# Optimization experiments

Hardware: AMD Instinct MI355X
Metric: run time of the kernel (lower is better)

Reference implementation:

```python
import jax, jax.numpy as jnp
import numpy as np

B, T, D = 8, 1024, 768
H, HD = 12, 64
DFF = 3072
EPS = 1e-5


def setup_inputs() -> dict:
    key = jax.random.key(0)
    ks = jax.random.split(key, 6)
    s = lambda fan_in: 1.0 / np.sqrt(fan_in)
    return {
        "x": jax.random.normal(ks[0], (B, T, D), jnp.float32),
        "ln1_g": jnp.ones((D,), jnp.float32),
        "ln1_b": jnp.zeros((D,), jnp.float32),
        "w_qkv": jax.random.normal(ks[1], (D, 3 * D), jnp.float32) * s(D),
        "b_qkv": jnp.zeros((3 * D,), jnp.float32),
        "w_out": jax.random.normal(ks[2], (D, D), jnp.float32) * s(D),
        "b_out": jnp.zeros((D,), jnp.float32),
        "ln2_g": jnp.ones((D,), jnp.float32),
        "ln2_b": jnp.zeros((D,), jnp.float32),
        "w_fc1": jax.random.normal(ks[3], (D, DFF), jnp.float32) * s(D),
        "b_fc1": jnp.zeros((DFF,), jnp.float32),
        "w_fc2": jax.random.normal(ks[4], (DFF, D), jnp.float32) * s(DFF),
        "b_fc2": jnp.zeros((D,), jnp.float32),
    }


def _layernorm(x, g, b):
    mu = jnp.mean(x, axis=-1, keepdims=True)
    var = jnp.var(x, axis=-1, keepdims=True)
    return (x - mu) * jax.lax.rsqrt(var + EPS) * g + b


def reference(x, ln1_g, ln1_b, w_qkv, b_qkv, w_out, b_out,
              ln2_g, ln2_b, w_fc1, b_fc1, w_fc2, b_fc2):
    # --- attention branch (pre-norm) ---
    h = _layernorm(x, ln1_g, ln1_b)
    qkv = h @ w_qkv + b_qkv                      # [B,T,3D]
    q, k, v = jnp.split(qkv, 3, axis=-1)
    # [B,T,D] -> [B,H,T,HD]
    re = lambda t: t.reshape(B, T, H, HD).transpose(0, 2, 1, 3)
    q, k, v = re(q), re(k), re(v)
    scores = jnp.einsum("bhqd,bhkd->bhqk", q, k) * (1.0 / np.sqrt(HD))
    causal = jnp.tril(jnp.ones((T, T), bool))    # [T,T]
    scores = jnp.where(causal, scores, -jnp.inf)
    attn_weights = jax.nn.softmax(scores, axis=-1)  # [B,H,T,T]
    out = jnp.einsum("bhqk,bhkd->bhqd", attn_weights, v)
    out = out.transpose(0, 2, 1, 3).reshape(B, T, D)
    attn_out = out @ w_out + b_out
    x = x + attn_out
    # --- MLP branch (pre-norm) ---
    h2 = _layernorm(x, ln2_g, ln2_b)
    ff = jax.nn.gelu(h2 @ w_fc1 + b_fc1, approximate=False) @ w_fc2 + b_fc2
    x = x + ff
    return x, attn_weights
```

## Files before the change

kernel.cpp:

```cpp
#include <hip/hip_runtime.h>
#include <cstdint>
#include <cstddef>

namespace {

constexpr int Bb  = 8;
constexpr int Tt  = 1024;
constexpr int Dd  = 768;
constexpr int Hh  = 12;
constexpr int DFF = 3072;
constexpr int BT  = Bb * Tt;

typedef __attribute__((ext_vector_type(8))) short bf16x8;
typedef __attribute__((ext_vector_type(4))) short bf16x4;
typedef __attribute__((ext_vector_type(4))) float f32x4;

__device__ __forceinline__ short f2bf(float f) {
  union { float f; unsigned u; } v; v.f = f;
  unsigned r = v.u + 0x7fffu + ((v.u >> 16) & 1u);
  return (short)(r >> 16);
}
__device__ __forceinline__ float gelu_exact(float v) {
  return 0.5f * v * (1.0f + erff(v * 0.70710678118654752f));
}

#define MFMA16(a, b, c) __builtin_amdgcn_mfma_f32_16x16x32_bf16(a, b, c, 0, 0, 0)

__device__ __forceinline__ void gl_lds16(const short* g, short* l) {
  __builtin_amdgcn_global_load_lds(
      (const __attribute__((address_space(1))) unsigned int*)(g),
      (__attribute__((address_space(3))) unsigned int*)(l), 16, 0, 0);
}

__global__ __launch_bounds__(256) void cvt_t(const float* __restrict__ in,
                                             short* __restrict__ out,
                                             int K, int N) {
  __shared__ float tile[32][33];
  int k0 = blockIdx.x * 32, n0 = blockIdx.y * 32;
  int tx = threadIdx.x & 31, ty = threadIdx.x >> 5;
  #pragma unroll
  for (int r = ty; r < 32; r += 8)
    tile[r][tx] = in[(size_t)(k0 + r) * N + n0 + tx];
  __syncthreads();
  #pragma unroll
  for (int r = ty; r < 32; r += 8)
    out[(size_t)(n0 + r) * K + k0 + tx] = f2bf(tile[tx][r]);
}

__global__ __launch_bounds__(256) void ln_rows(const float* __restrict__ x,
                                               const float* __restrict__ g,
                                               const float* __restrict__ b,
                                               short* __restrict__ out) {
  int lane = threadIdx.x & 63, wid = threadIdx.x >> 6;
  int row = blockIdx.x * 4 + wid;
  const float* xr = x + (size_t)row * Dd;
  float v[12];
  float s = 0.f, ss = 0.f;
  #pragma unroll
  for (int c = 0; c < 3; c++) {
    float4 t = *(const float4*)&xr[c * 256 + lane * 4];
    v[c * 4 + 0] = t.x; v[c * 4 + 1] = t.y; v[c * 4 + 2] = t.z; v[c * 4 + 3] = t.w;
    s  += t.x + t.y + t.z + t.w;
    ss += t.x * t.x + t.y * t.y + t.z * t.z + t.w * t.w;
  }
  #pragma unroll
  for (int off = 1; off < 64; off <<= 1) {
    s += __shfl_xor(s, off); ss += __shfl_xor(ss, off);
  }
  float mu   = s * (1.f / Dd);
  float var  = ss * (1.f / Dd) - mu * mu;
  float rstd = rsqrtf(var + 1e-5f);
  #pragma unroll
  for (int c = 0; c < 3; c++) {
    bf16x4 o;
    #pragma unroll
    for (int j = 0; j < 4; j++) {
      int d = c * 256 + lane * 4 + j;
      o[j] = f2bf((v[c * 4 + j] - mu) * rstd * g[d] + b[d]);
    }
    *(bf16x4*)&out[(size_t)row * Dd + c * 256 + lane * 4] = o;
  }
}

template <int EPI, int N, bool VTR>
__global__ __launch_bounds__(256) void gemm_bt(const short* __restrict__ A,
                                               const short* __restrict__ Bt,
                                               const float* __restrict__ bias,
                                               const float* __restrict__ add,
                                               void* __restrict__ outp,
                                               int K,
                                               short* __restrict__ vt) {
  __shared__ short S[17408];
  short* As0 = S;
  short* As1 = S + 4096;
  short* Bs0 = S + 8192;
  short* Bs1 = S + 12288;

  int nbx = gridDim.x;
  int flat = blockIdx.y * nbx + blockIdx.x;
  int cpx = (nbx * gridDim.y) >> 3;
  int swz = (flat & 7) * cpx + (flat >> 3);
  int m0 = (swz % nbx) * 128, n0 = (swz / nbx) * 128;

  int tid = threadIdx.x;
  int lane = tid & 63, wid = tid >> 6;
  int wm = wid >> 1, wn = wid & 1;
  int l15 = lane & 15, lg = lane >> 4;

  int jr = tid >> 2, jc = (tid & 3) << 3;
  int ldsb = wid << 9;

  auto stage = [&](short* Ad, short* Bd, int k0) {
    gl_lds16(&A[(size_t)(m0 + jr) * K + k0 + jc],       Ad + ldsb);
    gl_lds16(&A[(size_t)(m0 + 64 + jr) * K + k0 + jc],  Ad + 2048 + ldsb);
    gl_lds16(&Bt[(size_t)(n0 + jr) * K + k0 + jc],      Bd + ldsb);
    gl_lds16(&Bt[(size_t)(n0 + 64 + jr) * K + k0 + jc], Bd + 2048 + ldsb);
  };

  f32x4 acc[4][4] = {};
  stage(As0, Bs0, 0);
  int nk = K >> 5;
  for (int t = 0; t < nk; ++t) {
    short* Ab = (t & 1) ? As1 : As0;
    short* Bb = (t & 1) ? Bs1 : Bs0;
    if (t + 1 < nk) {
      stage((t & 1) ? As0 : As1, (t & 1) ? Bs0 : Bs1, (t + 1) << 5);
      asm volatile("s_waitcnt vmcnt(4)" ::: "memory");
    } else {
      asm volatile("s_waitcnt vmcnt(0)" ::: "memory");
    }
    __syncthreads();
    bf16x8 af[4], bfr[4];
    #pragma unroll
    for (int i = 0; i < 4; i++) af[i]  = *(bf16x8*)&Ab[(wm * 64 + i * 16 + l15) * 32 + lg * 8];
    #pragma unroll
    for (int j = 0; j < 4; j++) bfr[j] = *(bf16x8*)&Bb[(wn * 64 + j * 16 + l15) * 32 + lg * 8];
    #pragma unroll
    for (int i = 0; i < 4; i++)
      #pragma unroll
      for (int j = 0; j < 4; j++)
        acc[i][j] = MFMA16(af[i], bfr[j], acc[i][j]);
    __syncthreads();
  }

  if (EPI == 0 || EPI == 2) {
    short (*Cl)[136] = (short (*)[136])S;
    #pragma unroll
    for (int i = 0; i < 4; i++)
      #pragma unroll
      for (int j = 0; j < 4; j++)
        #pragma unroll
        for (int r = 0; r < 4; r++) {
          int row = wm * 64 + i * 16 + lg * 4 + r;
          int col = wn * 64 + j * 16 + l15;
          float vv = acc[i][j][r] + bias[n0 + col];
          if (EPI == 2) vv = gelu_exact(vv);
          int ch = col >> 3, co = col & 7;
          Cl[row][((ch ^ (row & 7)) << 3) | co] = f2bf(vv);
        }
    __syncthreads();
    if (VTR && n0 >= 1536) {
      int b = m0 >> 10, tbase = m0 & 1023;
      int h0 = (n0 - 1536) >> 6;
      #pragma unroll
      for (int half = 0; half < 2; ++half) {
        int c = (tid >> 2) + half * 64;
        int hh = c >> 6, d = c & 63;
        short* dst = vt + ((size_t)((b * Hh + h0 + hh) * 64 + d)) * Tt
                        + tbase + (tid & 3) * 32;
        #pragma unroll
        for (int j = 0; j < 4; ++j) {
          bf16x8 v8;
          #pragma unroll
          for (int k = 0; k < 8; ++k) {
            int t = (tid & 3) * 32 + j * 8 + k;
            v8[k] = Cl[t][(((c >> 3) ^ (t & 7)) << 3) | (c & 7)];
          }
          *(bf16x8*)(dst + j * 8) = v8;
        }
      }
    } else {
      int row = tid >> 1;
      int cb = (tid & 1) * 8;
      #pragma unroll
      for (int c = 0; c < 8; c++) {
        int ch = cb + c;
        bf16x8 v8 = *(bf16x8*)&Cl[row][(ch ^ (row & 7)) << 3];
        *(bf16x8*)&((short*)outp)[(size_t)(m0 + row) * N + n0 + (ch << 3)] = v8;
      }
    }
  } else {
    #pragma unroll
    for (int i = 0; i < 4; i++)
      #pragma unroll
      for (int j = 0; j < 4; j++)
        #pragma unroll
        for (int r = 0; r < 4; r++) {
          int m = m0 + wm * 64 + i * 16 + lg * 4 + r;
          int n = n0 + wn * 64 + j * 16 + l15;
          float vv = acc[i][j][r] + bias[n];
          size_t idx = (size_t)m * N + n;
          float ov = vv + add[idx];
          if (EPI == 3) __builtin_nontemporal_store(ov, &((float*)outp)[idx]);
          else          ((float*)outp)[idx] = ov;
        }
  }
}

template <int EPI>
__global__ __launch_bounds__(256) void gemm_n64(const short* __restrict__ A,
                                                const short* __restrict__ Bt,
                                                const float* __restrict__ bias,
                                                const float* __restrict__ add,
                                                float* __restrict__ outp,
                                                int K) {
  constexpr int N = 768;
  __shared__ short S[12288];
  short* As0 = S;
  short* As1 = S + 2048;
  short* Bs0 = S + 4096;
  short* Bs1 = S + 8192;

  int nbx = gridDim.x;
  int flat = blockIdx.y * nbx + blockIdx.x;
  int cpx = (nbx * gridDim.y) >> 3;
  int swz = (flat & 7) * cpx + (flat >> 3);
  int m0 = (swz % nbx) * 64, n0 = (swz / nbx) * 128;

  int tid = threadIdx.x;
  int lane = tid & 63, wid = tid >> 6;
  int wm = wid & 1, wn = wid >> 1;
  int l15 = lane & 15, lg = lane >> 4;

  int jr = tid >> 2, jc = (tid & 3) << 3;
  int ldsb = wid << 9;

  auto stage = [&](short* Ad, short* Bd, int k0) {
    gl_lds16(&A[(size_t)(m0 + jr) * K + k0 + jc],       Ad + ldsb);
    gl_lds16(&Bt[(size_t)(n0 + jr) * K + k0 + jc],      Bd + ldsb);
    gl_lds16(&Bt[(size_t)(n0 + 64 + jr) * K + k0 + jc], Bd + 2048 + ldsb);
  };

  f32x4 acc[2][4] = {};
  stage(As0, Bs0, 0);
  int nk = K >> 5;
  for (int t = 0; t < nk; ++t) {
    short* Ab = (t & 1) ? As1 : As0;
    short* Bb = (t & 1) ? Bs1 : Bs0;
    if (t + 1 < nk) {
      stage((t & 1) ? As0 : As1, (t & 1) ? Bs0 : Bs1, (t + 1) << 5);
      asm volatile("s_waitcnt vmcnt(3)" ::: "memory");
    } else {
      asm volatile("s_waitcnt vmcnt(0)" ::: "memory");
    }
    __syncthreads();
    bf16x8 af[2], bfr[4];
    #pragma unroll
    for (int i = 0; i < 2; i++) af[i]  = *(bf16x8*)&Ab[(wm * 32 + i * 16 + l15) * 32 + lg * 8];
    #pragma unroll
    for (int j = 0; j < 4; j++) bfr[j] = *(bf16x8*)&Bb[(wn * 64 + j * 16 + l15) * 32 + lg * 8];
    #pragma unroll
    for (int i = 0; i < 2; i++)
      #pragma unroll
      for (int j = 0; j < 4; j++)
        acc[i][j] = MFMA16(af[i], bfr[j], acc[i][j]);
    __syncthreads();
  }

  #pragma unroll
  for (int i = 0; i < 2; i++)
    #pragma unroll
    for (int j = 0; j < 4; j++)
      #pragma unroll
      for (int r = 0; r < 4; r++) {
        int m = m0 + wm * 32 + i * 16 + lg * 4 + r;
        int n = n0 + wn * 64 + j * 16 + l15;
        float vv = acc[i][j][r] + bias[n];
        size_t idx = (size_t)m * N + n;
        float ov = vv + add[idx];
        if (EPI == 3) __builtin_nontemporal_store(ov, &outp[idx]);
        else          outp[idx] = ov;
      }
}

__global__ __launch_bounds__(256) void attn_fused(const short* __restrict__ qkv,
                                                  const short* __restrict__ vt,
                                                  float* __restrict__ attw,
                                                  short* __restrict__ ctx) {
  __shared__ short VtL[2][4096];
  __shared__ float Pf[4][16][68];
  int flat = blockIdx.y * 16 + blockIdx.x;
  int xcd = flat & 7, rr0 = flat >> 3;
  int bh   = xcd * 12 + (rr0 >> 4);
  int tile = 15 - (rr0 & 15);
  int q0 = tile * 64;
  int b = bh / Hh, h = bh % Hh;
  int tid = threadIdx.x, lane = tid & 63, wid = tid >> 6;
  int l15 = lane & 15, lg = lane >> 4;
  const short* base = qkv + (size_t)b * Tt * 2304;

  bf16x8 qa[2];
  {
    const short* qp = base + (size_t)(q0 + wid * 16 + l15) * 2304 + h * 64 + lg * 8;
    qa[0] = *(const bf16x8*)qp;
    qa[1] = *(const bf16x8*)(qp + 32);
  }

  float l[4] = {0.f, 0.f, 0.f, 0.f};
  for (int kt = 0; kt <= tile; ++kt) {
    f32x4 acc[4] = {};
    #pragma unroll
    for (int nf = 0; nf < 4; ++nf) {
      const short* kp = base + (size_t)(kt * 64 + nf * 16 + l15) * 2304 + 768 + h * 64 + lg * 8;
      bf16x8 k0 = *(const bf16x8*)kp;
      bf16x8 k1 = *(const bf16x8*)(kp + 32);
      acc[nf] = MFMA16(qa[0], k0, acc[nf]);
      acc[nf] = MFMA16(qa[1], k1, acc[nf]);
    }
    #pragma unroll
    for (int r = 0; r < 4; r++) {
      int qg = q0 + wid * 16 + lg * 4 + r;
      #pragma unroll
      for (int nf = 0; nf < 4; nf++) {
        int kg = kt * 64 + nf * 16 + l15;
        l[r] += (kg <= qg) ? __expf(acc[nf][r] * 0.125f) : 0.f;
      }
    }
  }
  float rl[4];
  #pragma unroll
  for (int r = 0; r < 4; r++) {
    float s = l[r];
    #pragma unroll
    for (int off = 1; off < 16; off <<= 1) s += __shfl_xor(s, off);
    rl[r] = 1.f / s;
  }

  const short* vtb = vt + (size_t)bh * 64 * Tt;
  int dS = wid * 16 + (lane >> 3);
  int cS = (lane & 7) ^ (lane >> 3);
  auto stageV = [&](int bi, int kt) {
    gl_lds16(&vtb[(size_t)dS * Tt + kt * 64 + cS * 8],       &VtL[bi][wid * 1024]);
    gl_lds16(&vtb[(size_t)(dS + 8) * Tt + kt * 64 + cS * 8], &VtL[bi][wid * 1024 + 512]);
  };

  f32x4 oacc[4] = {};
  stageV(0, 0);
  for (int kt = 0; kt <= tile; ++kt) {
    int cur = kt & 1;
    f32x4 acc[4] = {};
    #pragma unroll
    for (int nf = 0; nf < 4; nf++) {
      const short* kp = base + (size_t)(kt * 64 + nf * 16 + l15) * 2304 + 768 + h * 64 + lg * 8;
      bf16x8 k0 = *(const bf16x8*)kp;
      bf16x8 k1 = *(const bf16x8*)(kp + 32);
      acc[nf] = MFMA16(qa[0], k0, acc[nf]);
      acc[nf] = MFMA16(qa[1], k1, acc[nf]);
    }
    #pragma unroll
    for (int nf = 0; nf < 4; nf++) {
      #pragma unroll
      for (int r = 0; r < 4; r++) {
        int qg = q0 + wid * 16 + lg * 4 + r;
        int kg = kt * 64 + nf * 16 + l15;
        float p = (kg <= qg) ? __expf(acc[nf][r] * 0.125f) * rl[r] : 0.f;
        Pf[wid][lg * 4 + r][nf * 16 + l15] = p;
      }
    }
    asm volatile("s_waitcnt lgkmcnt(0)" ::: "memory");
    __builtin_amdgcn_sched_barrier(0);
    #pragma unroll
    for (int it = 0; it < 4; ++it) {
      int pr = it * 4 + lg;
      f32x4 pv = *(f32x4*)&Pf[wid][pr][l15 * 4];
      __builtin_nontemporal_store(
          pv, (f32x4*)&attw[((size_t)bh * Tt + q0 + wid * 16 + pr) * Tt + kt * 64 + l15 * 4]);
    }
    f32x4 pf0 = *(f32x4*)&Pf[wid][l15][lg * 8];
    f32x4 pf1 = *(f32x4*)&Pf[wid][l15][lg * 8 + 4];
    f32x4 pf2 = *(f32x4*)&Pf[wid][l15][lg * 8 + 32];
    f32x4 pf3 = *(f32x4*)&Pf[wid][l15][lg * 8 + 36];
    bf16x8 pa0, pa1;
    #pragma unroll
    for (int j = 0; j < 4; j++) {
      pa0[j] = f2bf(pf0[j]); pa0[4 + j] = f2bf(pf1[j]);
      pa1[j] = f2bf(pf2[j]); pa1[4 + j] = f2bf(pf3[j]);
    }
    asm volatile("s_waitcnt vmcnt(4)" ::: "memory");
    __builtin_amdgcn_s_barrier();
    __builtin_amdgcn_sched_barrier(0);
    if (kt < tile) stageV(cur ^ 1, kt + 1);
    #pragma unroll
    for (int nf = 0; nf < 4; nf++) {
      int dA = nf * 16 + l15;
      int sw = dA & 7;
      bf16x8 vb0 = *(bf16x8*)&VtL[cur][dA * 64 + ((lg ^ sw) << 3)];
      bf16x8 vb1 = *(bf16x8*)&VtL[cur][dA * 64 + (((4 + lg) ^ sw) << 3)];
      oacc[nf] = MFMA16(pa0, vb0, oacc[nf]);
      oacc[nf] = MFMA16(pa1, vb1, oacc[nf]);
    }
  }
  f32x4 z = {0.f, 0.f, 0.f, 0.f};
  for (int kt = tile + 1; kt < 16; ++kt) {
    #pragma unroll
    for (int it = 0; it < 4; ++it) {
      int pr = it * 4 + lg;
      __builtin_nontemporal_store(
          z, (f32x4*)&attw[((size_t)bh * Tt + q0 + wid * 16 + pr) * Tt + kt * 64 + l15 * 4]);
    }
  }
  #pragma unroll
  for (int nf = 0; nf < 4; nf++) {
    #pragma unroll
    for (int r = 0; r < 4; r++) {
      int t = q0 + wid * 16 + lg * 4 + r;
      ctx[((size_t)b * Tt + t) * Dd + h * 64 + nf * 16 + l15] = f2bf(oacc[nf][r]);
    }
  }
}

}

extern "C" void kernel_launch(void* const* d_in, const int* in_sizes, int n_in,
                              void* d_out, int out_size, void* d_ws, size_t ws_size,
                              hipStream_t stream) {
  const float* x     = (const float*)d_in[0];
  const float* ln1g  = (const float*)d_in[1];
  const float* ln1b  = (const float*)d_in[2];
  const float* w_qkv = (const float*)d_in[3];
  const float* b_qkv = (const float*)d_in[4];
  const float* w_out = (const float*)d_in[5];
  const float* b_out = (const float*)d_in[6];
  const float* ln2g  = (const float*)d_in[7];
  const float* ln2b  = (const float*)d_in[8];
  const float* w_fc1 = (const float*)d_in[9];
  const float* b_fc1 = (const float*)d_in[10];
  const float* w_fc2 = (const float*)d_in[11];
  const float* b_fc2 = (const float*)d_in[12];

  char* ws = (char*)d_ws;
  size_t o = 0;
  short* wqkvT = (short*)(ws + o); o += (size_t)2304 * 768 * 2;
  short* woutT = (short*)(ws + o); o += (size_t)768 * 768 * 2;
  short* wfc1T = (short*)(ws + o); o += (size_t)3072 * 768 * 2;
  short* wfc2T = (short*)(ws + o); o += (size_t)768 * 3072 * 2;
  short* h     = (short*)(ws + o); o += (size_t)BT * Dd * 2;
  short* qkv   = (short*)(ws + o); o += (size_t)BT * 2304 * 2;
  float* y1    = (float*)(ws + o); o += (size_t)BT * Dd * 4;
  short* h2    = (short*)(ws + o); o += (size_t)BT * Dd * 2;
  short* vt    = (short*)(ws + o); o += (size_t)96 * 64 * Tt * 2;
  short* ctx  = h;
  short* gbuf = h;

  float* out_x = (float*)d_out;
  float* attw  = out_x + (size_t)BT * Dd;

  cvt_t<<<dim3(768 / 32, 2304 / 32), 256, 0, stream>>>(w_qkv, wqkvT, 768, 2304);
  cvt_t<<<dim3(768 / 32, 768 / 32),  256, 0, stream>>>(w_out, woutT, 768, 768);
  cvt_t<<<dim3(768 / 32, 3072 / 32), 256, 0, stream>>>(w_fc1, wfc1T, 768, 3072);
  cvt_t<<<dim3(3072 / 32, 768 / 32), 256, 0, stream>>>(w_fc2, wfc2T, 3072, 768);

  ln_rows<<<BT / 4, 256, 0, stream>>>(x, ln1g, ln1b, h);
  gemm_bt<0, 2304, true><<<dim3(BT / 128, 2304 / 128), 256, 0, stream>>>(
      h, wqkvT, b_qkv, nullptr, qkv, 768, vt);
  attn_fused<<<dim3(16, 96), 256, 0, stream>>>(qkv, vt, attw, ctx);
  gemm_n64<1><<<dim3(BT / 64, 768 / 128), 256, 0, stream>>>(ctx, woutT, b_out, x, y1, 768);
  ln_rows<<<BT / 4, 256, 0, stream>>>(y1, ln2g, ln2b, h2);
  gemm_bt<2, 3072, false><<<dim3(BT / 128, 3072 / 128), 256, 0, stream>>>(
      h2, wfc1T, b_fc1, nullptr, gbuf, 768, nullptr);
  gemm_n64<3><<<dim3(BT / 64, 768 / 128), 256, 0, stream>>>(gbuf, wfc2T, b_fc2, y1, out_x, 3072);
}
```

Measured before the change: 427.3 us.

## Merge weight conversion and first layernorm into one launch; use K=64 tiles for FC2 GEMM

Folds the four weight transpose-convert kernels and the first layernorm into a single prep kernel that dispatches work by block index, cutting four launches and their tail gaps. Adds a new FC2 GEMM variant that stages 64-wide K slices per iteration instead of the previous depth. This halves the number of barrier-separated steps over K=3072. The cost is more LDS per block, which may lower occupancy.

```diff
diff --git a/kernel.cpp b/kernel.cpp
--- a/kernel.cpp
+++ b/kernel.cpp
@@ -32,11 +32,11 @@
       (__attribute__((address_space(3))) unsigned int*)(l), 16, 0, 0);
 }
 
-__global__ __launch_bounds__(256) void cvt_t(const float* __restrict__ in,
-                                             short* __restrict__ out,
-                                             int K, int N) {
-  __shared__ float tile[32][33];
-  int k0 = blockIdx.x * 32, n0 = blockIdx.y * 32;
+__device__ __forceinline__ void cvt_body(float (*tile)[33],
+                                         const float* __restrict__ in,
+                                         short* __restrict__ out,
+                                         int K, int N, int bx, int by) {
+  int k0 = bx * 32, n0 = by * 32;
   int tx = threadIdx.x & 31, ty = threadIdx.x >> 5;
   #pragma unroll
   for (int r = ty; r < 32; r += 8)
@@ -47,12 +47,12 @@
     out[(size_t)(n0 + r) * K + k0 + tx] = f2bf(tile[tx][r]);
 }
 
-__global__ __launch_bounds__(256) void ln_rows(const float* __restrict__ x,
-                                               const float* __restrict__ g,
-                                               const float* __restrict__ b,
-                                               short* __restrict__ out) {
+__device__ __forceinline__ void ln_body(const float* __restrict__ x,
+                                        const float* __restrict__ g,
+                                        const float* __restrict__ b,
+                                        short* __restrict__ out, int blkrow) {
   int lane = threadIdx.x & 63, wid = threadIdx.x >> 6;
-  int row = blockIdx.x * 4 + wid;
+  int row = blkrow * 4 + wid;
   const float* xr = x + (size_t)row * Dd;
   float v[12];
   float s = 0.f, ss = 0.f;
@@ -80,6 +80,30 @@
     }
     *(bf16x4*)&out[(size_t)row * Dd + c * 256 + lane * 4] = o;
   }
+}
+
+__global__ __launch_bounds__(256) void prep(const float* __restrict__ w_qkv, short* wqkvT,
+                                            const float* __restrict__ w_out, short* woutT,
+                                            const float* __restrict__ w_fc1, short* wfc1T,
+                                            const float* __restrict__ w_fc2, short* wfc2T,
+                                            const float* __restrict__ x,
+                                            const float* __restrict__ g,
+                                            const float* __restrict__ b,
+                                            short* __restrict__ h) {
+  __shared__ float tile[32][33];
+  int j = blockIdx.x;
+  if (j < 1728)      cvt_body(tile, w_qkv, wqkvT, 768, 2304, j % 24, j / 24);
+  else if (j < 2304) { int t = j - 1728; cvt_body(tile, w_out, woutT, 768, 768, t % 24, t / 24); }
+  else if (j < 4608) { int t = j - 2304; cvt_body(tile, w_fc1, wfc1T, 768, 3072, t % 24, t / 24); }
+  else if (j < 6912) { int t = j - 4608; cvt_body(tile, w_fc2, wfc2T, 3072, 768, t % 96, t / 96); }
+  else               ln_body(x, g, b, h, j - 6912);
+}
+
+__global__ __launch_bounds__(256) void ln_rows(const float* __restrict__ x,
+                                               const float* __restrict__ g,
+                                               const float* __restrict__ b,
+                                               short* __restrict__ out) {
+  ln_body(x, g, b, out, blockIdx.x);
 }
 
 template <int EPI, int N, bool VTR>
@@ -283,6 +307,98 @@
       }
 }
 
+template <int EPI>
+__global__ __launch_bounds__(256) void gemm_n64k64(const short* __restrict__ A,
+                                                   const short* __restrict__ Bt,
+                                                   const float* __restrict__ bias,
+                                                   const float* __restrict__ add,
+                                                   float* __restrict__ outp,
+                                                   int K) {
+  constexpr int N = 768;
+  __shared__ short S[24576];
+  short* As0 = S;
+  short* As1 = S + 4096;
+  short* Bs0 = S + 8192;
+  short* Bs1 = S + 16384;
+
+  int nbx = gridDim.x;
+  int flat = blockIdx.y * nbx + blockIdx.x;
+  int cpx = (nbx * gridDim.y) >> 3;
+  int swz = (flat & 7) * cpx + (flat >> 3);
+  int m0 = (swz % nbx) * 64, n0 = (swz / nbx) * 128;
+
+  int tid = threadIdx.x;
+  int lane = tid & 63, wid = tid >> 6;
+  int wm = wid & 1, wn = wid >> 1;
+  int l15 = lane & 15, lg = lane >> 4;
+
+  int r8 = tid >> 3;
+  int gsl = (tid & 7) ^ (r8 & 7);
+  int wb = wid << 9;
+
+  auto stage = [&](short* Ad, short* Bd, int k0) {
+    #pragma unroll
+    for (int c = 0; c < 2; ++c)
+      gl_lds16(&A[(size_t)(m0 + c * 32 + r8) * K + k0 + gsl * 8], Ad + c * 2048 + wb);
+    #pragma unroll
+    for (int c = 0; c < 4; ++c)
+      gl_lds16(&Bt[(size_t)(n0 + c * 32 + r8) * K + k0 + gsl * 8], Bd + c * 2048 + wb);
+  };
+
+  f32x4 acc[2][4] = {};
+  stage(As0, Bs0, 0);
+  int nk = K >> 6;
+  for (int t = 0; t < nk; ++t) {
+    short* Ab = (t & 1) ? As1 : As0;
+    short* Bb = (t & 1) ? Bs1 : Bs0;
+    if (t + 1 < nk) {
+      stage((t & 1) ? As0 : As1, (t & 1) ? Bs0 : Bs1, (t + 1) << 6);
+      asm volatile("s_waitcnt vmcnt(6)" ::: "memory");
+    } else {
+      asm volatile("s_waitcnt vmcnt(0)" ::: "memory");
+    }
+    __syncthreads();
+    bf16x8 af[2][2], bfr[4][2];
+    #pragma unroll
+    for (int i = 0; i < 2; i++) {
+      int r = wm * 32 + i * 16 + l15;
+      #pragma unroll
+      for (int kk = 0; kk < 2; kk++)
+        af[i][kk] = *(bf16x8*)&Ab[r * 64 + (((kk * 4 + lg) ^ (r & 7)) << 3)];
+    }
+    #pragma unroll
+    for (int j = 0; j < 4; j++) {
+      int r = wn * 64 + j * 16 + l15;
+      #pragma unroll
+      for (int kk = 0; kk < 2; kk++)
+        bfr[j][kk] = *(bf16x8*)&Bb[r * 64 + (((kk * 4 + lg) ^ (r & 7)) << 3)];
+    }
+    #pragma unroll
+    for (int kk = 0; kk < 2; kk++)
+      #pragma unroll
+      for (int i = 0; i < 2; i++)
+        #pragma unroll
+        for (int j = 0; j < 4; j++)
+          acc[i][j] = MFMA16(af[i][kk], bfr[j][kk], acc[i][j]);
+    __syncthreads();
+  }
+
+  #pragma unroll
+  for (int i = 0; i < 2; i++)
+    #pragma unroll
+    for (int j = 0; j < 4; j++)
+      #pragma unroll
+      for (int r = 0; r < 4; r++) {
+        int m = m0 + wm * 32 + i * 16 + lg * 4 + r;
+        int n = n0 + wn * 64 + j * 16 + l15;
+        float vv = acc[i][j][r] + bias[n];
+        size_t idx = (size_t)m * N + n;
+        float ov = vv + add[idx];
+        if (EPI == 3) __builtin_nontemporal_store(ov, &outp[idx]);
+        else          outp[idx] = ov;
+      }
+}
+
 __global__ __launch_bounds__(256) void attn_fused(const short* __restrict__ qkv,
                                                   const short* __restrict__ vt,
                                                   float* __restrict__ attw,
@@ -455,12 +571,8 @@
   float* out_x = (float*)d_out;
   float* attw  = out_x + (size_t)BT * Dd;
 
-  cvt_t<<<dim3(768 / 32, 2304 / 32), 256, 0, stream>>>(w_qkv, wqkvT, 768, 2304);
-  cvt_t<<<dim3(768 / 32, 768 / 32),  256, 0, stream>>>(w_out, woutT, 768, 768);
-  cvt_t<<<dim3(768 / 32, 3072 / 32), 256, 0, stream>>>(w_fc1, wfc1T, 768, 3072);
-  cvt_t<<<dim3(3072 / 32, 768 / 32), 256, 0, stream>>>(w_fc2, wfc2T, 3072, 768);
-
-  ln_rows<<<BT / 4, 256, 0, stream>>>(x, ln1g, ln1b, h);
+  prep<<<8960, 256, 0, stream>>>(w_qkv, wqkvT, w_out, woutT, w_fc1, wfc1T,
+                                 w_fc2, wfc2T, x, ln1g, ln1b, h);
   gemm_bt<0, 2304, true><<<dim3(BT / 128, 2304 / 128), 256, 0, stream>>>(
       h, wqkvT, b_qkv, nullptr, qkv, 768, vt);
   attn_fused<<<dim3(16, 96), 256, 0, stream>>>(qkv, vt, attw, ctx);
@@ -468,5 +580,5 @@
   ln_rows<<<BT / 4, 256, 0, stream>>>(y1, ln2g, ln2b, h2);
   gemm_bt<2, 3072, false><<<dim3(BT / 128, 3072 / 128), 256, 0, stream>>>(
       h2, wfc1T, b_fc1, nullptr, gbuf, 768, nullptr);
-  gemm_n64<3><<<dim3(BT / 64, 768 / 128), 256, 0, stream>>>(gbuf, wfc2T, b_fc2, y1, out_x, 3072);
-}
+  gemm_n64k64<3><<<dim3(BT / 64, 768 / 128), 256, 0, stream>>>(gbuf, wfc2T, b_fc2, y1, out_x, 3072);
+}
```

Result: faster. 405.9 us (-5.0%).
